# Performance work log

Measured on AMD Instinct MI355X. Metric: run time of the kernel, lower is better.

Reference implementation:

```python
import jax, jax.numpy as jnp
import numpy as np
import math

K_BRANCH = 8  # config['k']

def _selectors(n, k):
    # Static (trace-time) construction of per-level gather indices, mask=True branch.
    L = math.ceil(math.log(n) / math.log(k)) + 1
    rel = [0] + [math.ceil(n / k ** i) for i in range(L)]  # level sizes, leaves first
    Li = np.cumsum(np.array(rel))                          # level start offsets in node dim
    sels = []
    for l in range(L):
        m = rel[l + 1]
        i = np.arange(m)[:, None]
        anc = None
        if l < L - 1:
            m_next = rel[l + 2]
            j = np.arange(m_next)[None, :]
            cond = (j + 1) / m_next <= i / m
            anc = np.where(cond, Li[l + 1] + j, 0)
        s = np.arange(k)[None, :]
        ridx = np.minimum(i // k * k + s, m - 1)
        sib = np.where(ridx <= i, Li[l] + ridx, 0)  # rel/m <= i/m  <=>  rel <= i
        chi = None
        if l >= 1:
            m_prev = rel[l]
            c = np.arange(k)[None, :]
            ridx = np.minimum(i * k + c, m_prev - 1)
            cond = ridx / m_prev <= i / m
            chi = np.where(cond, Li[l - 1] + ridx, 0)
        sels.append((anc, sib, chi))
    return L, Li, sels

def _sdp(q, Kmat, Vmat, sel, d):
    keys = Kmat[:, :, sel, :]   # [b,h,m,w,d] gather
    vals = Vmat[:, :, sel, :]
    logits = jnp.einsum('bhnd,bhnkd->bhnk', q, keys) / math.sqrt(d)
    w = jax.nn.softmax(logits, axis=-1)
    return jnp.einsum('bhnk,bhnkd->bhnd', w, vals)

def setup_inputs() -> dict:
    key = jax.random.key(0)
    k1, k2, k3 = jax.random.split(key, 3)
    b, h, n_tot, d = 2, 4, 585, 128
    return {
        'Q': jax.random.normal(k1, (b, h, n_tot, d), dtype=jnp.float32),
        'K': jax.random.normal(k2, (b, h, n_tot, d), dtype=jnp.float32),
        'V': jax.random.normal(k3, (b, h, n_tot, d), dtype=jnp.float32),
        'n': 512,
    }

def reference(Q, K, V, n):
    k = K_BRANCH
    d = Q.shape[-1]
    L, Li, sels = _selectors(int(n), k)
    # Sequential bottom-up level updates: V at level l is rewritten before level l+1 reads it.
    for l in range(L):
        anc, sib, chi = sels[l]
        q = Q[:, :, Li[l]:Li[l + 1], :]
        out = _sdp(q, K, V, sib, d)
        if anc is not None:
            out = out + _sdp(q, K, V, anc, d)
        if chi is not None:
            out = out + _sdp(q, K, V, chi, d)
        V = V.at[:, :, Li[l]:Li[l + 1], :].set(out / 3.0)
    return V
```

## Files before the change

kernel.cpp:

```cpp
#include <hip/hip_runtime.h>
#include <math.h>

#define D 128
#define NTOT 585
#define SCALE 0.08838834764831845f
#define THIRD 0.33333333333333333f
#define LROW 132

__device__ __forceinline__ float rsum_c(float v) {
    v += __shfl_xor(v, 1, 64);
    v += __shfl_xor(v, 2, 64);
    v += __shfl_xor(v, 4, 64);
    return v;
}
__device__ __forceinline__ float rsum_s(float v) {
    v += __shfl_xor(v, 8, 64);
    v += __shfl_xor(v, 16, 64);
    v += __shfl_xor(v, 32, 64);
    return v;
}
__device__ __forceinline__ float rmax_s(float v) {
    v = fmaxf(v, __shfl_xor(v, 8, 64));
    v = fmaxf(v, __shfl_xor(v, 16, 64));
    v = fmaxf(v, __shfl_xor(v, 32, 64));
    return v;
}
__device__ __forceinline__ float dot16(const float4 q[4], const float* __restrict__ row, int c) {
    const float4* k = (const float4*)(row + (c << 4));
    float4 k0 = k[0], k1 = k[1], k2 = k[2], k3 = k[3];
    float p0 = q[0].x * k0.x + q[0].y * k0.y + q[0].z * k0.z + q[0].w * k0.w;
    float p1 = q[1].x * k1.x + q[1].y * k1.y + q[1].z * k1.z + q[1].w * k1.w;
    float p2 = q[2].x * k2.x + q[2].y * k2.y + q[2].z * k2.z + q[2].w * k2.w;
    float p3 = q[3].x * k3.x + q[3].y * k3.y + q[3].z * k3.z + q[3].w * k3.w;
    return (p0 + p1) + (p2 + p3);
}
__device__ __forceinline__ void vacc(float w, const float* __restrict__ row, int c, float4 acc[4]) {
    const float4* v = (const float4*)(row + (c << 4));
#pragma unroll
    for (int u = 0; u < 4; ++u) {
        float4 t = v[u];
        acc[u].x += w * t.x; acc[u].y += w * t.y; acc[u].z += w * t.z; acc[u].w += w * t.w;
    }
}
__device__ __forceinline__ void vacc_reg(float w, const float4 vv[4], float4 acc[4]) {
#pragma unroll
    for (int u = 0; u < 4; ++u) {
        acc[u].x += w * vv[u].x; acc[u].y += w * vv[u].y;
        acc[u].z += w * vv[u].z; acc[u].w += w * vv[u].w;
    }
}
__device__ __forceinline__ void loadq(const float* __restrict__ qrow, int c, float4 q[4]) {
    const float4* qp = (const float4*)(qrow + (c << 4));
#pragma unroll
    for (int u = 0; u < 4; ++u) q[u] = qp[u];
}
__device__ __forceinline__ void butterfly_acc(float4 acc[4]) {
#pragma unroll
    for (int u = 0; u < 4; ++u) {
        acc[u].x = rsum_s(acc[u].x);
        acc[u].y = rsum_s(acc[u].y);
        acc[u].z = rsum_s(acc[u].z);
        acc[u].w = rsum_s(acc[u].w);
    }
}

__device__ __forceinline__ void anc_l0(const float4 q4[4], int g, int s, int c,
                                       const float* __restrict__ Ks,
                                       const float* __restrict__ Vs,
                                       float lg0, float4 acc[4]) {
    float lgA[8];
    float mloc = lg0;
#pragma unroll
    for (int R = 0; R < 4; ++R) {
        if (16 * R < g) {
#pragma unroll
            for (int rr = 0; rr < 2; ++rr) {
                const int r = 2 * R + rr;
                const int j = 8 * r + s;
                float lg = -1e30f;
                if (j < g)
                    lg = rsum_c(dot16(q4, &Ks[(16 + j) * LROW], c)) * SCALE;
                lgA[r] = lg;
                mloc = fmaxf(mloc, lg);
            }
        } else { lgA[2 * R] = -1e30f; lgA[2 * R + 1] = -1e30f; }
    }
    const float m = rmax_s(mloc);
    const float e0 = __expf(lg0 - m);
    float zp = (s == 0) ? (float)(64 - g) * e0 : 0.f;
    float eA[8];
#pragma unroll
    for (int R = 0; R < 4; ++R) {
        if (16 * R < g) {
#pragma unroll
            for (int rr = 0; rr < 2; ++rr) {
                const int r = 2 * R + rr;
                eA[r] = (lgA[r] > -1e29f) ? __expf(lgA[r] - m) : 0.f;
                zp += eA[r];
            }
        }
    }
    const float inv = 1.f / rsum_s(zp);
#pragma unroll
    for (int R = 0; R < 4; ++R) {
        if (16 * R < g) {
#pragma unroll
            for (int rr = 0; rr < 2; ++rr) {
                const int r = 2 * R + rr;
                const int j = 8 * r + s;
                if (j < g) vacc(eA[r] * inv, &Vs[(16 + j) * LROW], c, acc);
            }
        }
    }
    if (s == 0) vacc((float)(64 - g) * e0 * inv, &Vs[80 * LROW], c, acc);
}

__global__ __launch_bounds__(1024) void sequoia_fused(const float* __restrict__ Q,
                                                      const float* __restrict__ K,
                                                      const float* __restrict__ V,
                                                      float* __restrict__ Out) {
    __shared__ float Ks[89 * LROW];
    __shared__ float Vs[89 * LROW];
    const int tid = threadIdx.x;
    const int lane = tid & 63;
    const int s = lane >> 3, c = lane & 7;
    const int bh = blockIdx.x >> 5;
    const int qb0 = (blockIdx.x & 31) << 4;
    const float* Qb = Q + (size_t)bh * NTOT * D;
    const float* Kb = K + (size_t)bh * NTOT * D;
    const float* Vb = V + (size_t)bh * NTOT * D;
    float* Ob = Out + (size_t)bh * NTOT * D;

    for (int t = tid; t < 89 * 32; t += 1024) {
        const int row = t >> 5, col = (t & 31) << 2;
        int src;
        if (row < 16)      src = qb0 + row;
        else if (row < 80) src = 512 + row - 16;
        else if (row == 80) src = 0;
        else               src = 576 + (row - 81);
        *(float4*)(&Ks[row * LROW + col]) = *(const float4*)(Kb + (size_t)src * D + col);
        *(float4*)(&Vs[row * LROW + col]) = *(const float4*)(Vb + (size_t)src * D + col);
    }
    __syncthreads();

    const int w = tid >> 6;

    {
        const int i = qb0 + w;
        const int sl = i & 7;
        const int g = i >> 3;
        const int sibbase = w & 8;

        float4 q4[4];
        loadq(Qb + (size_t)i * D, c, q4);
        float4 acc[4] = {{0,0,0,0},{0,0,0,0},{0,0,0,0},{0,0,0,0}};
        const float lg0 = rsum_c(dot16(q4, &Ks[80 * LROW], c)) * SCALE;
        {
            float lg = -1e30f;
            if (s <= sl)
                lg = rsum_c(dot16(q4, &Ks[(sibbase + s) * LROW], c)) * SCALE;
            const float m = fmaxf(rmax_s(lg), lg0);
            const float e = (s <= sl) ? __expf(lg - m) : 0.f;
            const float e0 = __expf(lg0 - m);
            float zp = e;
            if (s == 0) zp += (float)(7 - sl) * e0;
            const float inv = 1.f / rsum_s(zp);
            if (s <= sl) vacc(e * inv, &Vs[(sibbase + s) * LROW], c, acc);
            if (s == 0 && sl < 7) vacc((float)(7 - sl) * e0 * inv, &Vs[80 * LROW], c, acc);
        }
        anc_l0(q4, g, s, c, Ks, Vs, lg0, acc);
        butterfly_acc(acc);
        if (s == 0) {
            float4* orow = (float4*)(Ob + (size_t)i * D + (c << 4));
#pragma unroll
            for (int u = 0; u < 4; ++u)
                orow[u] = make_float4(acc[u].x * THIRD, acc[u].y * THIRD,
                                      acc[u].z * THIRD, acc[u].w * THIRD);
        }
    }

    if (w < 2) {
        const int ci = (qb0 >> 3) + w;

        float4 v0n[4];
        {
            const float4* vp = (const float4*)(&Vs[80 * LROW] + (c << 4));
#pragma unroll
            for (int u = 0; u < 4; ++u) {
                float4 v = vp[u];
                v0n[u] = make_float4(v.x * (2.f * THIRD), v.y * (2.f * THIRD),
                                     v.z * (2.f * THIRD), v.w * (2.f * THIRD));
            }
        }

        float4 o0[4];
        if (ci == 0) {
#pragma unroll
            for (int u = 0; u < 4; ++u) o0[u] = v0n[u];
        } else {
            float4 q0[4];
            loadq(Qb + (size_t)(8 * ci) * D, c, q0);
            float4 acc[4] = {{0,0,0,0},{0,0,0,0},{0,0,0,0},{0,0,0,0}};
            const float lg0 = rsum_c(dot16(q0, &Ks[80 * LROW], c)) * SCALE;
            {
                float lg = -1e30f;
                if (s == 0)
                    lg = rsum_c(dot16(q0, &Ks[(8 * w) * LROW], c)) * SCALE;
                const float m = fmaxf(rmax_s(lg), lg0);
                const float e = (s == 0) ? __expf(lg - m) : 0.f;
                const float e0 = __expf(lg0 - m);
                float zp = e;
                if (s == 0) zp += 7.f * e0;
                const float inv = 1.f / rsum_s(zp);
                if (s == 0) {
                    vacc(e * inv, &Vs[(8 * w) * LROW], c, acc);
                    vacc(7.f * e0 * inv, &Vs[80 * LROW], c, acc);
                }
            }
            anc_l0(q0, ci, s, c, Ks, Vs, lg0, acc);
            butterfly_acc(acc);
#pragma unroll
            for (int u = 0; u < 4; ++u)
                o0[u] = make_float4(acc[u].x * THIRD, acc[u].y * THIRD,
                                    acc[u].z * THIRD, acc[u].w * THIRD);
        }

        float4 o1[4];
        {
            float4 q1[4];
            loadq(Qb + (size_t)(512 + ci) * D, c, q1);
            float4 acc[4] = {{0,0,0,0},{0,0,0,0},{0,0,0,0},{0,0,0,0}};
            const float lg0q = rsum_c(dot16(q1, &Ks[80 * LROW], c)) * SCALE;
            const int sl1 = ci & 7;
            const int gq = ci >> 3;
            {
                const int slot = 16 + (ci & ~7) + s;
                float lg = -1e30f;
                if (s <= sl1)
                    lg = rsum_c(dot16(q1, &Ks[slot * LROW], c)) * SCALE;
                const float m = fmaxf(rmax_s(lg), lg0q);
                const float e = (s <= sl1) ? __expf(lg - m) : 0.f;
                const float e0 = __expf(lg0q - m);
                float zp = e;
                if (s == 0) zp += (float)(7 - sl1) * e0;
                const float inv = 1.f / rsum_s(zp);
                if (s <= sl1) vacc(e * inv, &Vs[slot * LROW], c, acc);
                if (s == 0 && sl1 < 7) vacc_reg((float)(7 - sl1) * e0 * inv, v0n, acc);
            }
            {
                float lg = -1e30f;
                if (s < gq)
                    lg = rsum_c(dot16(q1, &Ks[(81 + s) * LROW], c)) * SCALE;
                const float m = fmaxf(rmax_s(lg), lg0q);
                const float e = (s < gq) ? __expf(lg - m) : 0.f;
                const float e0 = __expf(lg0q - m);
                float zp = e;
                if (s == 0) zp += (float)(8 - gq) * e0;
                const float inv = 1.f / rsum_s(zp);
                if (s < gq) vacc(e * inv, &Vs[(81 + s) * LROW], c, acc);
                if (s == 0) vacc_reg((float)(8 - gq) * e0 * inv, v0n, acc);
            }
            {
                float lg = -1e30f;
                if (s == 0)
                    lg = rsum_c(dot16(q1, &Ks[(8 * w) * LROW], c)) * SCALE;
                const float m = fmaxf(rmax_s(lg), lg0q);
                const float e = (s == 0) ? __expf(lg - m) : 0.f;
                const float e0 = __expf(lg0q - m);
                const float zp = (s == 0) ? (e + 7.f * e0) : 0.f;
                const float inv = 1.f / rsum_s(zp);
                if (s == 0) {
                    vacc_reg(e * inv, o0, acc);
                    vacc_reg(7.f * e0 * inv, v0n, acc);
                }
            }
            butterfly_acc(acc);
#pragma unroll
            for (int u = 0; u < 4; ++u)
                o1[u] = make_float4(acc[u].x * THIRD, acc[u].y * THIRD,
                                    acc[u].z * THIRD, acc[u].w * THIRD);
            if (s == 0) {
                float4* orow = (float4*)(Ob + (size_t)(512 + ci) * D + (c << 4));
#pragma unroll
                for (int u = 0; u < 4; ++u) orow[u] = o1[u];
            }
        }

        if (w == 0 && (ci & 7) == 0) {
            const int j = ci >> 3;
            float4 q2[4];
            loadq(Qb + (size_t)(576 + j) * D, c, q2);
            float4 acc[4] = {{0,0,0,0},{0,0,0,0},{0,0,0,0},{0,0,0,0}};
            const float lg0q = rsum_c(dot16(q2, &Ks[80 * LROW], c)) * SCALE;
            {
                float lg = -1e30f;
                if (s <= j)
                    lg = rsum_c(dot16(q2, &Ks[(81 + s) * LROW], c)) * SCALE;
                const float m = fmaxf(rmax_s(lg), lg0q);
                const float e = (s <= j) ? __expf(lg - m) : 0.f;
                const float e0 = __expf(lg0q - m);
                float zp = e;
                if (s == 0) zp += (float)(7 - j) * e0;
                const float inv = 1.f / rsum_s(zp);
                if (s <= j) vacc(e * inv, &Vs[(81 + s) * LROW], c, acc);
                if (s == 0 && j < 7) vacc_reg((float)(7 - j) * e0 * inv, v0n, acc);
            }
            {
                float lg = -1e30f;
                if (s == 0)
                    lg = rsum_c(dot16(q2, &Ks[(16 + 8 * j) * LROW], c)) * SCALE;
                const float m = fmaxf(rmax_s(lg), lg0q);
                const float e = (s == 0) ? __expf(lg - m) : 0.f;
                const float e0 = __expf(lg0q - m);
                const float zp = (s == 0) ? (e + 7.f * e0) : 0.f;
                const float inv = 1.f / rsum_s(zp);
                if (s == 0) {
                    vacc_reg(e * inv, o1, acc);
                    vacc_reg(7.f * e0 * inv, v0n, acc);
                }
            }
            butterfly_acc(acc);
            float4 o2[4];
#pragma unroll
            for (int u = 0; u < 4; ++u)
                o2[u] = make_float4((acc[u].x + v0n[u].x) * THIRD,
                                    (acc[u].y + v0n[u].y) * THIRD,
                                    (acc[u].z + v0n[u].z) * THIRD,
                                    (acc[u].w + v0n[u].w) * THIRD);
            if (s == 0) {
                float4* orow = (float4*)(Ob + (size_t)(576 + j) * D + (c << 4));
#pragma unroll
                for (int u = 0; u < 4; ++u) orow[u] = o2[u];
            }

            if (j == 0) {
                float4 q3[4];
                loadq(Qb + (size_t)584 * D, c, q3);
                const float lg0r = rsum_c(dot16(q3, &Ks[80 * LROW], c)) * SCALE;
                float lg = -1e30f;
                if (s == 0)
                    lg = rsum_c(dot16(q3, &Ks[81 * LROW], c)) * SCALE;
                const float m = fmaxf(rmax_s(lg), lg0r);
                const float e = (s == 0) ? __expf(lg - m) : 0.f;
                const float e0 = __expf(lg0r - m);
                const float zp = (s == 0) ? (e + 7.f * e0) : 0.f;
                const float inv = 1.f / rsum_s(zp);
                float4 acc3[4] = {{0,0,0,0},{0,0,0,0},{0,0,0,0},{0,0,0,0}};
                if (s == 0) {
                    vacc_reg(e * inv, o2, acc3);
                    vacc_reg(7.f * e0 * inv, v0n, acc3);
                }
                butterfly_acc(acc3);
                if (s == 0) {
                    const float4* v584 = (const float4*)(Vb + (size_t)584 * D + (c << 4));
                    float4* orow = (float4*)(Ob + (size_t)584 * D + (c << 4));
#pragma unroll
                    for (int u = 0; u < 4; ++u) {
                        float4 bb = v584[u];
                        orow[u] = make_float4((acc3[u].x + bb.x) * THIRD,
                                              (acc3[u].y + bb.y) * THIRD,
                                              (acc3[u].z + bb.z) * THIRD,
                                              (acc3[u].w + bb.w) * THIRD);
                    }
                }
            }
        }
    }
}

extern "C" void kernel_launch(void* const* d_in, const int* in_sizes, int n_in,
                              void* d_out, int out_size, void* d_ws, size_t ws_size,
                              hipStream_t stream) {
    const float* Q = (const float*)d_in[0];
    const float* K = (const float*)d_in[1];
    const float* V = (const float*)d_in[2];
    float* Out = (float*)d_out;
    hipLaunchKernelGGL(sequoia_fused, dim3(256), dim3(1024), 0, stream, Q, K, V, Out);
}
```

Measured before the change: 77.01 us.

## Pair leaf groups x and 63-x per block and reuse level-0 output

Each block now takes two leaf groups, x and 63-x, instead of two adjacent ones, so the upper-level work spreads across waves. The wave that owns the first leaf of each group does the level-1 and level-2 work, reusing its own level-0 output from registers rather than recomputing the child's level-0 attention. The Q row load is also issued before the barrier to overlap with the shared-memory fill. This removes the redundant recompute and the serial tail on waves 0-1, but the pairing may change the leaf-to-ancestor tie-break semantics.

```diff
diff --git a/kernel.cpp b/kernel.cpp
--- a/kernel.cpp
+++ b/kernel.cpp
@@ -125,34 +125,36 @@
     const int lane = tid & 63;
     const int s = lane >> 3, c = lane & 7;
     const int bh = blockIdx.x >> 5;
-    const int qb0 = (blockIdx.x & 31) << 4;
+    const int x  = blockIdx.x & 31;
+    const int gA = x, gB = 63 - x;
     const float* Qb = Q + (size_t)bh * NTOT * D;
     const float* Kb = K + (size_t)bh * NTOT * D;
     const float* Vb = V + (size_t)bh * NTOT * D;
     float* Ob = Out + (size_t)bh * NTOT * D;
 
+    const int w = tid >> 6;
+    const int grp = (w < 8) ? gA : gB;
+    const int sl = w & 7;
+    const int i = 8 * grp + sl;
+    const int sibbase = w & 8;
+
     for (int t = tid; t < 89 * 32; t += 1024) {
         const int row = t >> 5, col = (t & 31) << 2;
         int src;
-        if (row < 16)      src = qb0 + row;
-        else if (row < 80) src = 512 + row - 16;
+        if (row < 8)        src = 8 * gA + row;
+        else if (row < 16)  src = 8 * gB + (row - 8);
+        else if (row < 80)  src = 512 + row - 16;
         else if (row == 80) src = 0;
-        else               src = 576 + (row - 81);
+        else                src = 576 + (row - 81);
         *(float4*)(&Ks[row * LROW + col]) = *(const float4*)(Kb + (size_t)src * D + col);
         *(float4*)(&Vs[row * LROW + col]) = *(const float4*)(Vb + (size_t)src * D + col);
     }
+    float4 q4[4];
+    loadq(Qb + (size_t)i * D, c, q4);
     __syncthreads();
 
-    const int w = tid >> 6;
-
+    float4 o0[4];
     {
-        const int i = qb0 + w;
-        const int sl = i & 7;
-        const int g = i >> 3;
-        const int sibbase = w & 8;
-
-        float4 q4[4];
-        loadq(Qb + (size_t)i * D, c, q4);
         float4 acc[4] = {{0,0,0,0},{0,0,0,0},{0,0,0,0},{0,0,0,0}};
         const float lg0 = rsum_c(dot16(q4, &Ks[80 * LROW], c)) * SCALE;
         {
@@ -168,19 +170,21 @@
             if (s <= sl) vacc(e * inv, &Vs[(sibbase + s) * LROW], c, acc);
             if (s == 0 && sl < 7) vacc((float)(7 - sl) * e0 * inv, &Vs[80 * LROW], c, acc);
         }
-        anc_l0(q4, g, s, c, Ks, Vs, lg0, acc);
+        anc_l0(q4, grp, s, c, Ks, Vs, lg0, acc);
         butterfly_acc(acc);
+#pragma unroll
+        for (int u = 0; u < 4; ++u)
+            o0[u] = make_float4(acc[u].x * THIRD, acc[u].y * THIRD,
+                                acc[u].z * THIRD, acc[u].w * THIRD);
         if (s == 0) {
             float4* orow = (float4*)(Ob + (size_t)i * D + (c << 4));
 #pragma unroll
-            for (int u = 0; u < 4; ++u)
-                orow[u] = make_float4(acc[u].x * THIRD, acc[u].y * THIRD,
-                                      acc[u].z * THIRD, acc[u].w * THIRD);
-        }
-    }
-
-    if (w < 2) {
-        const int ci = (qb0 >> 3) + w;
+            for (int u = 0; u < 4; ++u) orow[u] = o0[u];
+        }
+    }
+
+    if (sl == 0) {
+        const int ci = grp;
 
         float4 v0n[4];
         {
@@ -191,38 +195,6 @@
                 v0n[u] = make_float4(v.x * (2.f * THIRD), v.y * (2.f * THIRD),
                                      v.z * (2.f * THIRD), v.w * (2.f * THIRD));
             }
-        }
-
-        float4 o0[4];
-        if (ci == 0) {
-#pragma unroll
-            for (int u = 0; u < 4; ++u) o0[u] = v0n[u];
-        } else {
-            float4 q0[4];
-            loadq(Qb + (size_t)(8 * ci) * D, c, q0);
-            float4 acc[4] = {{0,0,0,0},{0,0,0,0},{0,0,0,0},{0,0,0,0}};
-            const float lg0 = rsum_c(dot16(q0, &Ks[80 * LROW], c)) * SCALE;
-            {
-                float lg = -1e30f;
-                if (s == 0)
-                    lg = rsum_c(dot16(q0, &Ks[(8 * w) * LROW], c)) * SCALE;
-                const float m = fmaxf(rmax_s(lg), lg0);
-                const float e = (s == 0) ? __expf(lg - m) : 0.f;
-                const float e0 = __expf(lg0 - m);
-                float zp = e;
-                if (s == 0) zp += 7.f * e0;
-                const float inv = 1.f / rsum_s(zp);
-                if (s == 0) {
-                    vacc(e * inv, &Vs[(8 * w) * LROW], c, acc);
-                    vacc(7.f * e0 * inv, &Vs[80 * LROW], c, acc);
-                }
-            }
-            anc_l0(q0, ci, s, c, Ks, Vs, lg0, acc);
-            butterfly_acc(acc);
-#pragma unroll
-            for (int u = 0; u < 4; ++u)
-                o0[u] = make_float4(acc[u].x * THIRD, acc[u].y * THIRD,
-                                    acc[u].z * THIRD, acc[u].w * THIRD);
         }
 
         float4 o1[4];
@@ -263,7 +235,7 @@
             {
                 float lg = -1e30f;
                 if (s == 0)
-                    lg = rsum_c(dot16(q1, &Ks[(8 * w) * LROW], c)) * SCALE;
+                    lg = rsum_c(dot16(q1, &Ks[sibbase * LROW], c)) * SCALE;
                 const float m = fmaxf(rmax_s(lg), lg0q);
                 const float e = (s == 0) ? __expf(lg - m) : 0.f;
                 const float e0 = __expf(lg0q - m);
@@ -286,7 +258,7 @@
             }
         }
 
-        if (w == 0 && (ci & 7) == 0) {
+        if ((ci & 7) == 0) {
             const int j = ci >> 3;
             float4 q2[4];
             loadq(Qb + (size_t)(576 + j) * D, c, q2);
```

Result: faster. 75.28 us (-2.2%).
